# Performance work log

Hardware: AMD Instinct MI355X
Metric: run time of the kernel (lower is better)

Reference implementation:

```python
import jax, jax.numpy as jnp
import numpy as np

D_MODEL = 256
N_HEADS = 8
D_FFN = 1024
B, N = 4, 1024
HEAD_DIM = D_MODEL // N_HEADS
LN_EPS = 1e-5


def _ln(x, g, b):
    mu = jnp.mean(x, axis=-1, keepdims=True)
    var = jnp.var(x, axis=-1, keepdims=True)
    return (x - mu) * jax.lax.rsqrt(var + LN_EPS) * g + b


def setup_inputs() -> dict:
    key = jax.random.key(0)
    ks = jax.random.split(key, 16)
    s = 0.02
    return {
        "embed": jax.random.normal(ks[0], (B, N, D_MODEL), jnp.float32),
        "refer_bbox": jax.random.uniform(ks[1], (B, N, 4), jnp.float32),
        "dist": jax.random.uniform(ks[2], (B, N, N), jnp.float32),
        "query_pos": jax.random.normal(ks[3], (B, N, D_MODEL), jnp.float32),
        "in_proj_w": jax.random.normal(ks[4], (3 * D_MODEL, D_MODEL), jnp.float32) * s,
        "in_proj_b": jnp.zeros((3 * D_MODEL,), jnp.float32),
        "out_w": jax.random.normal(ks[5], (D_MODEL, D_MODEL), jnp.float32) * s,
        "out_b": jnp.zeros((D_MODEL,), jnp.float32),
        "tau_w": jax.random.normal(ks[6], (N_HEADS, D_MODEL), jnp.float32) * s,
        "tau_b": jax.random.uniform(ks[7], (N_HEADS,), jnp.float32, 0.0, 2.0),
        "w1": jax.random.normal(ks[8], (D_FFN, D_MODEL), jnp.float32) * s,
        "b1": jnp.zeros((D_FFN,), jnp.float32),
        "w2": jax.random.normal(ks[9], (D_MODEL, D_FFN), jnp.float32) * s,
        "b2": jnp.zeros((D_MODEL,), jnp.float32),
        "g1": jnp.ones((D_MODEL,), jnp.float32),
        "beta1": jnp.zeros((D_MODEL,), jnp.float32),
        "g2": jnp.ones((D_MODEL,), jnp.float32),
        "beta2": jnp.zeros((D_MODEL,), jnp.float32),
    }


def reference(embed, refer_bbox, dist, query_pos, in_proj_w, in_proj_b, out_w, out_b,
              tau_w, tau_b, w1, b1, w2, b2, g1, beta1, g2, beta2):
    # tau: (B, N, H) -> (B, H, N); additive bias mask[b,h,i,j] = dist[b,i,j] * tau[b,h,i]
    tau = (embed @ tau_w.T + tau_b).transpose(0, 2, 1)
    bias = dist[:, None, :, :] * tau[..., None]  # (B, H, N, N)

    qk = embed + query_pos  # q = k = embed + pos, v = embed
    wq, wk, wv = jnp.split(in_proj_w, 3, axis=0)
    bq, bk, bv = jnp.split(in_proj_b, 3, axis=0)
    q = (qk @ wq.T + bq).reshape(B, N, N_HEADS, HEAD_DIM)
    k = (qk @ wk.T + bk).reshape(B, N, N_HEADS, HEAD_DIM)
    v = (embed @ wv.T + bv).reshape(B, N, N_HEADS, HEAD_DIM)

    scores = jnp.einsum("bihd,bjhd->bhij", q, k) / np.sqrt(HEAD_DIM) + bias
    attn = jax.nn.softmax(scores, axis=-1)
    ctx = jnp.einsum("bhij,bjhd->bihd", attn, v).reshape(B, N, D_MODEL)
    tgt = ctx @ out_w.T + out_b

    x = _ln(embed + tgt, g1, beta1)
    ffn = jax.nn.relu(x @ w1.T + b1) @ w2.T + b2
    return _ln(x + ffn, g2, beta2)
```

## Files before the change

### kernel.cpp

```cpp
#include <hip/hip_runtime.h>
#include <math.h>

#define D_MODEL 256
#define N_HEADS 8
#define HEAD_DIM 32
#define D_FFN   1024
#define BB      4
#define NN      1024
#define M_TOT   (BB * NN)
#define LN_EPS  1e-5f

#define QSCALE_LOG2E 0.2550348612f
#define LOG2E        1.4426950408889634f

typedef float f32x4 __attribute__((ext_vector_type(4)));
typedef short bf16x8 __attribute__((ext_vector_type(8)));

__device__ __forceinline__ unsigned short f2bf(float f) {
    unsigned int u = __float_as_uint(f);
    unsigned int r = (u + 0x7fffu + ((u >> 16) & 1u)) >> 16;
    return (unsigned short)r;
}
__device__ __forceinline__ ushort4 pack4(float4 v) {
    ushort4 o; o.x = f2bf(v.x); o.y = f2bf(v.y); o.z = f2bf(v.z); o.w = f2bf(v.w);
    return o;
}
__device__ __forceinline__ float fast_exp2(float x) {
#if __has_builtin(__builtin_amdgcn_exp2f)
    return __builtin_amdgcn_exp2f(x);
#else
    return exp2f(x);
#endif
}

__global__ __launch_bounds__(256)
void prep_all_kernel(const float4* __restrict__ e, const float4* __restrict__ qp,
                     ushort4* __restrict__ ebf, ushort4* __restrict__ qkbf,
                     const float4* __restrict__ inw, const float4* __restrict__ outw,
                     const float4* __restrict__ w1, const float4* __restrict__ w2,
                     const float4* __restrict__ tauw,
                     ushort4* __restrict__ o_inw, ushort4* __restrict__ o_outw,
                     ushort4* __restrict__ o_w1, ushort4* __restrict__ o_w2,
                     ushort4* __restrict__ o_taupad) {
    if (blockIdx.x < 1024) {
        int i = blockIdx.x * 256 + threadIdx.x;
        float4 ev = e[i], pv = qp[i];
        ebf[i] = pack4(ev);
        float4 s = make_float4(ev.x + pv.x, ev.y + pv.y, ev.z + pv.z, ev.w + pv.w);
        qkbf[i] = pack4(s);
    } else {
        int i = (blockIdx.x - 1024) * 256 + threadIdx.x;
        if (i < 49152)       o_inw[i] = pack4(inw[i]);
        else if (i < 65536)  o_outw[i - 49152] = pack4(outw[i - 49152]);
        else if (i < 131072) o_w1[i - 65536] = pack4(w1[i - 65536]);
        else if (i < 196608) o_w2[i - 131072] = pack4(w2[i - 131072]);
        else if (i < 200704) {
            int q = i - 196608;
            if (q < 512) o_taupad[q] = pack4(tauw[q]);
            else { ushort4 z = {0, 0, 0, 0}; o_taupad[q] = z; }
        }
    }
}

__global__ __launch_bounds__(256)
void qkv_mfma_kernel(const unsigned short* __restrict__ qk_bf,
                     const unsigned short* __restrict__ emb_bf,
                     const unsigned short* __restrict__ inw_bf,
                     const unsigned short* __restrict__ taupad,
                     const float* __restrict__ in_proj_b, const float* __restrict__ tau_b,
                     unsigned short* __restrict__ qb, unsigned short* __restrict__ kb,
                     unsigned short* __restrict__ vbT, float* __restrict__ taub) {
    const int w    = threadIdx.x >> 6;
    const int lane = threadIdx.x & 63;
    const int l16 = lane & 15, l4 = lane >> 4;
    const int n0 = blockIdx.x * 64;
    const int m0 = blockIdx.y * 64;
    const int wm = (w >> 1) * 32, wn = (w & 1) * 32;

    const unsigned short* A = (blockIdx.x < 8) ? qk_bf : emb_bf;
    const unsigned short* W0 = (n0 < 768) ? &inw_bf[(size_t)(n0 + wn + l16) * D_MODEL]
                                          : &taupad[(size_t)(wn + l16) * D_MODEL];
    const unsigned short* Ar0 = &A[(size_t)(m0 + wm + l16) * D_MODEL];

    f32x4 acc[2][2] = {};
    #pragma unroll
    for (int k0 = 0; k0 < D_MODEL; k0 += 32) {
        bf16x8 a0 = *(const bf16x8*)&Ar0[k0 + l4 * 8];
        bf16x8 a1 = *(const bf16x8*)&Ar0[16 * D_MODEL + k0 + l4 * 8];
        bf16x8 b0 = *(const bf16x8*)&W0[k0 + l4 * 8];
        bf16x8 b1 = *(const bf16x8*)&W0[16 * D_MODEL + k0 + l4 * 8];
        acc[0][0] = __builtin_amdgcn_mfma_f32_16x16x32_bf16(a0, b0, acc[0][0], 0, 0, 0);
        acc[0][1] = __builtin_amdgcn_mfma_f32_16x16x32_bf16(a0, b1, acc[0][1], 0, 0, 0);
        acc[1][0] = __builtin_amdgcn_mfma_f32_16x16x32_bf16(a1, b0, acc[1][0], 0, 0, 0);
        acc[1][1] = __builtin_amdgcn_mfma_f32_16x16x32_bf16(a1, b1, acc[1][1], 0, 0, 0);
    }

    #pragma unroll
    for (int i = 0; i < 2; i++) {
        #pragma unroll
        for (int j = 0; j < 2; j++) {
            #pragma unroll
            for (int r = 0; r < 4; r++) {
                const int m = m0 + wm + i * 16 + l4 * 4 + r;
                const int b = m >> 10, nrow = m & 1023;
                const int c = n0 + wn + j * 16 + l16;
                float v = acc[i][j][r];
                if (c < 256) {
                    v = (v + in_proj_b[c]) * QSCALE_LOG2E;
                    int h = c >> 5, d = c & 31;
                    qb[((size_t)(b * N_HEADS + h) * NN + nrow) * HEAD_DIM + d] = f2bf(v);
                } else if (c < 512) {
                    v += in_proj_b[c];
                    int cc = c - 256; int h = cc >> 5, d = cc & 31;
                    kb[((size_t)(b * N_HEADS + h) * NN + nrow) * HEAD_DIM + d] = f2bf(v);
                } else if (c < 768) {
                    v += in_proj_b[c];
                    int cc = c - 512; int h = cc >> 5, d = cc & 31;
                    vbT[((size_t)(b * N_HEADS + h) * HEAD_DIM + d) * NN + nrow] = f2bf(v);
                } else if (c < 776) {
                    v = (v + tau_b[c - 768]) * LOG2E;
                    taub[(size_t)(b * N_HEADS + (c - 768)) * NN + nrow] = v;
                }
            }
        }
    }
}

__global__ __launch_bounds__(256)
void attn_mfma_kernel(const unsigned short* __restrict__ qb,
                      const unsigned short* __restrict__ kb,
                      const unsigned short* __restrict__ vbT,
                      const float* __restrict__ taub,
                      const float* __restrict__ dist,
                      float* __restrict__ Opart,
                      float* __restrict__ lpart) {
    __shared__ unsigned short Plds[4][16 * 72];
    const int w    = threadIdx.x >> 6;
    const int lane = threadIdx.x & 63;
    const int l16  = lane & 15;
    const int l4   = lane >> 4;
    const int bh = blockIdx.y;
    const int b = bh >> 3;
    const int z = blockIdx.z;
    const int i0 = blockIdx.x * 64 + w * 16;
    const int jbase = z * 256;

    const f32x4 zero = {0.f, 0.f, 0.f, 0.f};
    bf16x8 qf = *(const bf16x8*)&qb[((size_t)bh * NN + i0 + l16) * HEAD_DIM + l4 * 8];

    float tau_r[4];
    const float* drow[4];
    #pragma unroll
    for (int r = 0; r < 4; r++) {
        tau_r[r] = taub[(size_t)bh * NN + i0 + l4 * 4 + r];
        drow[r] = &dist[((size_t)b * NN + i0 + l4 * 4 + r) * NN];
    }

    float l_acc[4] = {0.f, 0.f, 0.f, 0.f};
    f32x4 O0 = zero, O1 = zero;

    unsigned short* pw = &Plds[w][0];
    const unsigned short* kbase = &kb[(size_t)bh * NN * HEAD_DIM];
    const unsigned short* vbase = &vbT[(size_t)bh * HEAD_DIM * NN];

    bf16x8 kf[4];
    float dd[4][4];
    #pragma unroll
    for (int s = 0; s < 4; s++)
        kf[s] = *(const bf16x8*)&kbase[(size_t)(jbase + s * 16 + l16) * HEAD_DIM + l4 * 8];
    #pragma unroll
    for (int s = 0; s < 4; s++)
        #pragma unroll
        for (int r = 0; r < 4; r++)
            dd[s][r] = drow[r][jbase + s * 16 + l16];

    for (int kt = 0; kt < 4; kt++) {
        const int j0 = jbase + kt * 64;
        bf16x8 vf[2][2];
        #pragma unroll
        for (int c = 0; c < 2; c++) {
            vf[c][0] = *(const bf16x8*)&vbase[(size_t)l16 * NN + j0 + c * 32 + l4 * 8];
            vf[c][1] = *(const bf16x8*)&vbase[(size_t)(16 + l16) * NN + j0 + c * 32 + l4 * 8];
        }
        bf16x8 kf_n[4];
        float dd_n[4][4];
        if (kt < 3) {
            const int j1 = j0 + 64;
            #pragma unroll
            for (int s = 0; s < 4; s++)
                kf_n[s] = *(const bf16x8*)&kbase[(size_t)(j1 + s * 16 + l16) * HEAD_DIM + l4 * 8];
            #pragma unroll
            for (int s = 0; s < 4; s++)
                #pragma unroll
                for (int r = 0; r < 4; r++)
                    dd_n[s][r] = drow[r][j1 + s * 16 + l16];
        }

        float parr[4][4];
        #pragma unroll
        for (int s = 0; s < 4; s++) {
            f32x4 S = __builtin_amdgcn_mfma_f32_16x16x32_bf16(qf, kf[s], zero, 0, 0, 0);
            #pragma unroll
            for (int r = 0; r < 4; r++) {
                const float p = fast_exp2(S[r] + dd[s][r] * tau_r[r]);
                parr[s][r] = p;
                l_acc[r] += p;
            }
        }

        #pragma unroll
        for (int s = 0; s < 4; s++)
            #pragma unroll
            for (int r = 0; r < 4; r++)
                pw[(l4 * 4 + r) * 72 + s * 16 + l16] = f2bf(parr[s][r]);
        asm volatile("s_waitcnt lgkmcnt(0)" ::: "memory");
        #pragma unroll
        for (int c = 0; c < 2; c++) {
            bf16x8 pf = *(const bf16x8*)&pw[l16 * 72 + c * 32 + l4 * 8];
            O0 = __builtin_amdgcn_mfma_f32_16x16x32_bf16(pf, vf[c][0], O0, 0, 0, 0);
            O1 = __builtin_amdgcn_mfma_f32_16x16x32_bf16(pf, vf[c][1], O1, 0, 0, 0);
        }

        if (kt < 3) {
            #pragma unroll
            for (int s = 0; s < 4; s++) {
                kf[s] = kf_n[s];
                #pragma unroll
                for (int r = 0; r < 4; r++) dd[s][r] = dd_n[s][r];
            }
        }
    }

    #pragma unroll
    for (int msk = 1; msk < 16; msk <<= 1)
        #pragma unroll
        for (int r = 0; r < 4; r++)
            l_acc[r] += __shfl_xor(l_acc[r], msk, 16);

    #pragma unroll
    for (int r = 0; r < 4; r++) {
        const int i = i0 + l4 * 4 + r;
        float* crow = &Opart[((size_t)(z * 32 + bh) * NN + i) * 32];
        crow[l16]      = O0[r];
        crow[16 + l16] = O1[r];
        if (l16 == 0)
            lpart[(size_t)(z * 32 + bh) * NN + i] = l_acc[r];
    }
}

__global__ __launch_bounds__(512)
void post_kernel(const float* __restrict__ Opart, const float* __restrict__ lpart,
                 const unsigned short* __restrict__ outw,
                 const float* __restrict__ out_b, const float* __restrict__ embed,
                 const float* __restrict__ g1, const float* __restrict__ beta1,
                 const unsigned short* __restrict__ w1, const float* __restrict__ b1,
                 const unsigned short* __restrict__ w2, const float* __restrict__ b2,
                 const float* __restrict__ g2, const float* __restrict__ beta2,
                 float* __restrict__ out) {
    __shared__ float Lh[16][8];
    __shared__ unsigned short cs[16][264];
    __shared__ unsigned short xs[16][264];
    __shared__ unsigned short fs[16][1032];
    __shared__ float sums[8][4][4][2];

    const int tid = threadIdx.x;
    const int w = tid >> 6, lane = tid & 63;
    const int l16 = lane & 15, l4 = lane >> 4;
    const int m0 = blockIdx.x * 16;
    const int b = m0 >> 10;

    if (tid < 128) {
        const int row = tid >> 3, h = tid & 7;
        const int i = (m0 + row) & 1023;
        const int rowA = ((b * 8 + h) << 10) + i;
        float l = 0.f;
        #pragma unroll
        for (int z = 0; z < 4; z++) l += lpart[z * 32768 + rowA];
        Lh[row][h] = 1.0f / l;
    }
    __syncthreads();

    {
        const int row = tid >> 5;
        const int d0 = (tid & 31) * 8;
        const int h = d0 >> 5;
        const int dd = d0 & 31;
        const int i = (m0 + row) & 1023;
        const int rowA = ((b * 8 + h) << 10) + i;
        f32x4 s0 = {0.f, 0.f, 0.f, 0.f}, s1 = {0.f, 0.f, 0.f, 0.f};
        #pragma unroll
        for (int z = 0; z < 4; z++) {
            const float* u = &Opart[((size_t)(z * 32768 + rowA)) * 32 + dd];
            s0 += *(const f32x4*)u;
            s1 += *(const f32x4*)(u + 4);
        }
        const float li = Lh[row][h];
        #pragma unroll
        for (int j = 0; j < 4; j++) {
            cs[row][d0 + j]     = f2bf(s0[j] * li);
            cs[row][d0 + 4 + j] = f2bf(s1[j] * li);
        }
    }
    __syncthreads();

    f32x4 accA[2] = {};
    #pragma unroll
    for (int k0 = 0; k0 < D_MODEL; k0 += 32) {
        bf16x8 a = *(const bf16x8*)&cs[l16][k0 + l4 * 8];
        #pragma unroll
        for (int j = 0; j < 2; j++) {
            const int c = w * 32 + j * 16 + l16;
            bf16x8 bj = *(const bf16x8*)&outw[(size_t)c * D_MODEL + k0 + l4 * 8];
            accA[j] = __builtin_amdgcn_mfma_f32_16x16x32_bf16(a, bj, accA[j], 0, 0, 0);
        }
    }
    float xv[2][4];
    {
        float s_r[4] = {0.f, 0.f, 0.f, 0.f}, q_r[4] = {0.f, 0.f, 0.f, 0.f};
        #pragma unroll
        for (int j = 0; j < 2; j++) {
            const int c = w * 32 + j * 16 + l16;
            const float bs = out_b[c];
            #pragma unroll
            for (int r = 0; r < 4; r++) {
                const int m = m0 + l4 * 4 + r;
                const float t = accA[j][r] + bs + embed[(size_t)m * D_MODEL + c];
                xv[j][r] = t; s_r[r] += t; q_r[r] += t * t;
            }
        }
        #pragma unroll
        for (int msk = 1; msk < 16; msk <<= 1)
            #pragma unroll
            for (int r = 0; r < 4; r++) {
                s_r[r] += __shfl_xor(s_r[r], msk, 16);
                q_r[r] += __shfl_xor(q_r[r], msk, 16);
            }
        if (l16 == 0)
            #pragma unroll
            for (int r = 0; r < 4; r++) {
                sums[w][l4][r][0] = s_r[r];
                sums[w][l4][r][1] = q_r[r];
            }
    }
    __syncthreads();
    #pragma unroll
    for (int r = 0; r < 4; r++) {
        float s = 0.f, q = 0.f;
        #pragma unroll
        for (int ww = 0; ww < 8; ww++) { s += sums[ww][l4][r][0]; q += sums[ww][l4][r][1]; }
        const float mu = s * (1.0f / D_MODEL);
        const float var = q * (1.0f / D_MODEL) - mu * mu;
        const float rstd = rsqrtf(var + LN_EPS);
        #pragma unroll
        for (int j = 0; j < 2; j++) {
            const int c = w * 32 + j * 16 + l16;
            const float ov = (xv[j][r] - mu) * rstd * g1[c] + beta1[c];
            xv[j][r] = ov;
            xs[l4 * 4 + r][c] = f2bf(ov);
        }
    }
    __syncthreads();

    f32x4 accB[8] = {};
    #pragma unroll
    for (int k0 = 0; k0 < D_MODEL; k0 += 32) {
        bf16x8 a = *(const bf16x8*)&xs[l16][k0 + l4 * 8];
        #pragma unroll
        for (int j = 0; j < 8; j++) {
            const int fc = w * 128 + j * 16 + l16;
            bf16x8 bj = *(const bf16x8*)&w1[(size_t)fc * D_MODEL + k0 + l4 * 8];
            accB[j] = __builtin_amdgcn_mfma_f32_16x16x32_bf16(a, bj, accB[j], 0, 0, 0);
        }
    }
    #pragma unroll
    for (int j = 0; j < 8; j++) {
        const int fc = w * 128 + j * 16 + l16;
        const float bs = b1[fc];
        #pragma unroll
        for (int r = 0; r < 4; r++)
            fs[l4 * 4 + r][fc] = f2bf(fmaxf(accB[j][r] + bs, 0.f));
    }
    __syncthreads();

    f32x4 accC[2] = {};
    #pragma unroll 8
    for (int k0 = 0; k0 < D_FFN; k0 += 32) {
        bf16x8 a = *(const bf16x8*)&fs[l16][k0 + l4 * 8];
        #pragma unroll
        for (int j = 0; j < 2; j++) {
            const int c = w * 32 + j * 16 + l16;
            bf16x8 bj = *(const bf16x8*)&w2[(size_t)c * D_FFN + k0 + l4 * 8];
            accC[j] = __builtin_amdgcn_mfma_f32_16x16x32_bf16(a, bj, accC[j], 0, 0, 0);
        }
    }
    float v2[2][4];
    {
        float s_r[4] = {0.f, 0.f, 0.f, 0.f}, q_r[4] = {0.f, 0.f, 0.f, 0.f};
        #pragma unroll
        for (int j = 0; j < 2; j++) {
            const int c = w * 32 + j * 16 + l16;
            const float bs = b2[c];
            #pragma unroll
            for (int r = 0; r < 4; r++) {
                const float t = accC[j][r] + bs + xv[j][r];
                v2[j][r] = t; s_r[r] += t; q_r[r] += t * t;
            }
        }
        #pragma unroll
        for (int msk = 1; msk < 16; msk <<= 1)
            #pragma unroll
            for (int r = 0; r < 4; r++) {
                s_r[r] += __shfl_xor(s_r[r], msk, 16);
                q_r[r] += __shfl_xor(q_r[r], msk, 16);
            }
        if (l16 == 0)
            #pragma unroll
            for (int r = 0; r < 4; r++) {
                sums[w][l4][r][0] = s_r[r];
                sums[w][l4][r][1] = q_r[r];
            }
    }
    __syncthreads();
    #pragma unroll
    for (int r = 0; r < 4; r++) {
        float s = 0.f, q = 0.f;
        #pragma unroll
        for (int ww = 0; ww < 8; ww++) { s += sums[ww][l4][r][0]; q += sums[ww][l4][r][1]; }
        const float mu = s * (1.0f / D_MODEL);
        const float var = q * (1.0f / D_MODEL) - mu * mu;
        const float rstd = rsqrtf(var + LN_EPS);
        const int m = m0 + l4 * 4 + r;
        #pragma unroll
        for (int j = 0; j < 2; j++) {
            const int c = w * 32 + j * 16 + l16;
            out[(size_t)m * D_MODEL + c] = (v2[j][r] - mu) * rstd * g2[c] + beta2[c];
        }
    }
}

extern "C" void kernel_launch(void* const* d_in, const int* in_sizes, int n_in,
                              void* d_out, int out_size, void* d_ws, size_t ws_size,
                              hipStream_t stream) {
    const float* embed     = (const float*)d_in[0];
    const float* dist      = (const float*)d_in[2];
    const float* query_pos = (const float*)d_in[3];
    const float* in_proj_w = (const float*)d_in[4];
    const float* in_proj_b = (const float*)d_in[5];
    const float* out_w     = (const float*)d_in[6];
    const float* out_b     = (const float*)d_in[7];
    const float* tau_w     = (const float*)d_in[8];
    const float* tau_b     = (const float*)d_in[9];
    const float* w1        = (const float*)d_in[10];
    const float* b1        = (const float*)d_in[11];
    const float* w2        = (const float*)d_in[12];
    const float* b2        = (const float*)d_in[13];
    const float* g1        = (const float*)d_in[14];
    const float* beta1     = (const float*)d_in[15];
    const float* g2        = (const float*)d_in[16];
    const float* beta2     = (const float*)d_in[17];
    float* out = (float*)d_out;

    char* ws = (char*)d_ws;
    const size_t MB = 1024 * 1024;
    const size_t KB = 1024;
    unsigned short* emb_bf  = (unsigned short*)(ws);
    unsigned short* qk_bf   = (unsigned short*)(ws + 2 * MB);
    unsigned short* qb      = (unsigned short*)(ws + 4 * MB);
    unsigned short* kb      = (unsigned short*)(ws + 6 * MB);
    unsigned short* vbT     = (unsigned short*)(ws + 8 * MB);
    float*          taub    = (float*)(ws + 10 * MB);
    unsigned short* inw_bf  = (unsigned short*)(ws + 11 * MB);
    unsigned short* outw_bf = (unsigned short*)(ws + 11 * MB + 512 * KB);
    unsigned short* w1_bf   = (unsigned short*)(ws + 12 * MB);
    unsigned short* w2_bf   = (unsigned short*)(ws + 12 * MB + 512 * KB);
    unsigned short* taupad  = (unsigned short*)(ws + 13 * MB);
    float*          Opart   = (float*)(ws + 14 * MB);
    float*          lpart   = (float*)(ws + 30 * MB);

    prep_all_kernel<<<dim3(1808), dim3(256), 0, stream>>>(
        (const float4*)embed, (const float4*)query_pos,
        (ushort4*)emb_bf, (ushort4*)qk_bf,
        (const float4*)in_proj_w, (const float4*)out_w, (const float4*)w1,
        (const float4*)w2, (const float4*)tau_w,
        (ushort4*)inw_bf, (ushort4*)outw_bf, (ushort4*)w1_bf, (ushort4*)w2_bf,
        (ushort4*)taupad);

    qkv_mfma_kernel<<<dim3(13, M_TOT / 64), dim3(256), 0, stream>>>(
        qk_bf, emb_bf, inw_bf, taupad, in_proj_b, tau_b, qb, kb, vbT, taub);

    attn_mfma_kernel<<<dim3(NN / 64, BB * N_HEADS, 4), dim3(256), 0, stream>>>(
        qb, kb, vbT, taub, dist, Opart, lpart);

    post_kernel<<<dim3(M_TOT / 16), dim3(512), 0, stream>>>(
        Opart, lpart, outw_bf, out_b, embed, g1, beta1,
        w1_bf, b1, w2_bf, b2, g2, beta2, out);
}
```

Measured before the change: 194.4 us.

## Fuse activation bf16 conversion into QKV GEMM, stage K/V in LDS, halve post tile

The separate embed/query_pos to bf16 pass is removed, and the QKV GEMM now reads fp32 activations and converts (and adds query_pos) in registers. The attention kernel cooperatively stages its K and V tiles in shared memory and permutes key order so the dist loads become vectorized float4, which drops the register double-buffering. The post kernel now processes 8 rows per block instead of 16, doubling the grid, and splits the K loops into two accumulators. The QKV GEMM converts redundantly across column blocks, and the 8-row post tile wastes half of each MFMA while re-reading the weights twice as often.

```diff
diff --git a/kernel.cpp b/kernel.cpp
--- a/kernel.cpp
+++ b/kernel.cpp
@@ -32,39 +32,46 @@
     return exp2f(x);
 #endif
 }
+__device__ __forceinline__ bf16x8 cvt8(const float* p) {
+    f32x4 x0 = *(const f32x4*)p, x1 = *(const f32x4*)(p + 4);
+    union { unsigned short s[8]; bf16x8 v; } u;
+    #pragma unroll
+    for (int j = 0; j < 4; j++) { u.s[j] = f2bf(x0[j]); u.s[4 + j] = f2bf(x1[j]); }
+    return u.v;
+}
+__device__ __forceinline__ bf16x8 cvt8_add(const float* p, const float* q) {
+    f32x4 x0 = *(const f32x4*)p, x1 = *(const f32x4*)(p + 4);
+    f32x4 y0 = *(const f32x4*)q, y1 = *(const f32x4*)(q + 4);
+    union { unsigned short s[8]; bf16x8 v; } u;
+    #pragma unroll
+    for (int j = 0; j < 4; j++) {
+        u.s[j] = f2bf(x0[j] + y0[j]);
+        u.s[4 + j] = f2bf(x1[j] + y1[j]);
+    }
+    return u.v;
+}
 
 __global__ __launch_bounds__(256)
-void prep_all_kernel(const float4* __restrict__ e, const float4* __restrict__ qp,
-                     ushort4* __restrict__ ebf, ushort4* __restrict__ qkbf,
-                     const float4* __restrict__ inw, const float4* __restrict__ outw,
-                     const float4* __restrict__ w1, const float4* __restrict__ w2,
-                     const float4* __restrict__ tauw,
-                     ushort4* __restrict__ o_inw, ushort4* __restrict__ o_outw,
-                     ushort4* __restrict__ o_w1, ushort4* __restrict__ o_w2,
-                     ushort4* __restrict__ o_taupad) {
-    if (blockIdx.x < 1024) {
-        int i = blockIdx.x * 256 + threadIdx.x;
-        float4 ev = e[i], pv = qp[i];
-        ebf[i] = pack4(ev);
-        float4 s = make_float4(ev.x + pv.x, ev.y + pv.y, ev.z + pv.z, ev.w + pv.w);
-        qkbf[i] = pack4(s);
-    } else {
-        int i = (blockIdx.x - 1024) * 256 + threadIdx.x;
-        if (i < 49152)       o_inw[i] = pack4(inw[i]);
-        else if (i < 65536)  o_outw[i - 49152] = pack4(outw[i - 49152]);
-        else if (i < 131072) o_w1[i - 65536] = pack4(w1[i - 65536]);
-        else if (i < 196608) o_w2[i - 131072] = pack4(w2[i - 131072]);
-        else if (i < 200704) {
-            int q = i - 196608;
-            if (q < 512) o_taupad[q] = pack4(tauw[q]);
-            else { ushort4 z = {0, 0, 0, 0}; o_taupad[q] = z; }
-        }
+void prep_w_kernel(const float4* __restrict__ inw, const float4* __restrict__ outw,
+                   const float4* __restrict__ w1, const float4* __restrict__ w2,
+                   const float4* __restrict__ tauw,
+                   ushort4* __restrict__ o_inw, ushort4* __restrict__ o_outw,
+                   ushort4* __restrict__ o_w1, ushort4* __restrict__ o_w2,
+                   ushort4* __restrict__ o_taupad) {
+    int i = blockIdx.x * 256 + threadIdx.x;
+    if (i < 49152)       o_inw[i] = pack4(inw[i]);
+    else if (i < 65536)  o_outw[i - 49152] = pack4(outw[i - 49152]);
+    else if (i < 131072) o_w1[i - 65536] = pack4(w1[i - 65536]);
+    else if (i < 196608) o_w2[i - 131072] = pack4(w2[i - 131072]);
+    else if (i < 200704) {
+        int q = i - 196608;
+        if (q < 512) o_taupad[q] = pack4(tauw[q]);
+        else { ushort4 z = {0, 0, 0, 0}; o_taupad[q] = z; }
     }
 }
 
 __global__ __launch_bounds__(256)
-void qkv_mfma_kernel(const unsigned short* __restrict__ qk_bf,
-                     const unsigned short* __restrict__ emb_bf,
+void qkv_mfma_kernel(const float* __restrict__ embed, const float* __restrict__ qpos,
                      const unsigned short* __restrict__ inw_bf,
                      const unsigned short* __restrict__ taupad,
                      const float* __restrict__ in_proj_b, const float* __restrict__ tau_b,
@@ -76,17 +83,21 @@
     const int n0 = blockIdx.x * 64;
     const int m0 = blockIdx.y * 64;
     const int wm = (w >> 1) * 32, wn = (w & 1) * 32;
-
-    const unsigned short* A = (blockIdx.x < 8) ? qk_bf : emb_bf;
+    const bool isqk = (blockIdx.x < 8);
+
+    const float* A0 = &embed[(size_t)(m0 + wm + l16) * D_MODEL];
+    const float* A1 = A0 + 16 * D_MODEL;
+    const float* P0 = &qpos[(size_t)(m0 + wm + l16) * D_MODEL];
+    const float* P1 = P0 + 16 * D_MODEL;
     const unsigned short* W0 = (n0 < 768) ? &inw_bf[(size_t)(n0 + wn + l16) * D_MODEL]
                                           : &taupad[(size_t)(wn + l16) * D_MODEL];
-    const unsigned short* Ar0 = &A[(size_t)(m0 + wm + l16) * D_MODEL];
 
     f32x4 acc[2][2] = {};
     #pragma unroll
     for (int k0 = 0; k0 < D_MODEL; k0 += 32) {
-        bf16x8 a0 = *(const bf16x8*)&Ar0[k0 + l4 * 8];
-        bf16x8 a1 = *(const bf16x8*)&Ar0[16 * D_MODEL + k0 + l4 * 8];
+        const int k = k0 + l4 * 8;
+        bf16x8 a0 = isqk ? cvt8_add(&A0[k], &P0[k]) : cvt8(&A0[k]);
+        bf16x8 a1 = isqk ? cvt8_add(&A1[k], &P1[k]) : cvt8(&A1[k]);
         bf16x8 b0 = *(const bf16x8*)&W0[k0 + l4 * 8];
         bf16x8 b1 = *(const bf16x8*)&W0[16 * D_MODEL + k0 + l4 * 8];
         acc[0][0] = __builtin_amdgcn_mfma_f32_16x16x32_bf16(a0, b0, acc[0][0], 0, 0, 0);
@@ -134,6 +145,8 @@
                       const float* __restrict__ dist,
                       float* __restrict__ Opart,
                       float* __restrict__ lpart) {
+    __shared__ unsigned short Kf[4][4][512];
+    __shared__ unsigned short Vf[4][2][2][512];
     __shared__ unsigned short Plds[4][16 * 72];
     const int w    = threadIdx.x >> 6;
     const int lane = threadIdx.x & 63;
@@ -145,89 +158,74 @@
     const int i0 = blockIdx.x * 64 + w * 16;
     const int jbase = z * 256;
 
+    {
+        const int kt = w;
+        const unsigned short* kb_z = &kb[((size_t)bh * NN + jbase + kt * 64) * HEAD_DIM];
+        #pragma unroll
+        for (int s = 0; s < 4; s++) {
+            bf16x8 kv = *(const bf16x8*)&kb_z[(size_t)(l16 * 4 + s) * HEAD_DIM + l4 * 8];
+            *(bf16x8*)&Kf[kt][s][lane * 8] = kv;
+        }
+        const unsigned short* vb_z = &vbT[(size_t)bh * HEAD_DIM * NN + jbase + kt * 64];
+        #pragma unroll
+        for (int c = 0; c < 2; c++)
+            #pragma unroll
+            for (int h2 = 0; h2 < 2; h2++) {
+                bf16x8 vv = *(const bf16x8*)&vb_z[(size_t)(h2 * 16 + l16) * NN + c * 32 + l4 * 8];
+                *(bf16x8*)&Vf[kt][c][h2][lane * 8] = vv;
+            }
+    }
+
     const f32x4 zero = {0.f, 0.f, 0.f, 0.f};
     bf16x8 qf = *(const bf16x8*)&qb[((size_t)bh * NN + i0 + l16) * HEAD_DIM + l4 * 8];
-
     float tau_r[4];
     const float* drow[4];
     #pragma unroll
     for (int r = 0; r < 4; r++) {
         tau_r[r] = taub[(size_t)bh * NN + i0 + l4 * 4 + r];
-        drow[r] = &dist[((size_t)b * NN + i0 + l4 * 4 + r) * NN];
-    }
-
+        drow[r] = &dist[((size_t)b * NN + i0 + l4 * 4 + r) * NN + jbase];
+    }
     float l_acc[4] = {0.f, 0.f, 0.f, 0.f};
     f32x4 O0 = zero, O1 = zero;
-
     unsigned short* pw = &Plds[w][0];
-    const unsigned short* kbase = &kb[(size_t)bh * NN * HEAD_DIM];
-    const unsigned short* vbase = &vbT[(size_t)bh * HEAD_DIM * NN];
-
-    bf16x8 kf[4];
-    float dd[4][4];
-    #pragma unroll
-    for (int s = 0; s < 4; s++)
-        kf[s] = *(const bf16x8*)&kbase[(size_t)(jbase + s * 16 + l16) * HEAD_DIM + l4 * 8];
-    #pragma unroll
-    for (int s = 0; s < 4; s++)
+
+    __syncthreads();
+
+    for (int kt = 0; kt < 4; kt++) {
+        const int j0 = kt * 64;
+        f32x4 dd4[4];
         #pragma unroll
         for (int r = 0; r < 4; r++)
-            dd[s][r] = drow[r][jbase + s * 16 + l16];
-
-    for (int kt = 0; kt < 4; kt++) {
-        const int j0 = jbase + kt * 64;
-        bf16x8 vf[2][2];
-        #pragma unroll
-        for (int c = 0; c < 2; c++) {
-            vf[c][0] = *(const bf16x8*)&vbase[(size_t)l16 * NN + j0 + c * 32 + l4 * 8];
-            vf[c][1] = *(const bf16x8*)&vbase[(size_t)(16 + l16) * NN + j0 + c * 32 + l4 * 8];
-        }
-        bf16x8 kf_n[4];
-        float dd_n[4][4];
-        if (kt < 3) {
-            const int j1 = j0 + 64;
-            #pragma unroll
-            for (int s = 0; s < 4; s++)
-                kf_n[s] = *(const bf16x8*)&kbase[(size_t)(j1 + s * 16 + l16) * HEAD_DIM + l4 * 8];
-            #pragma unroll
-            for (int s = 0; s < 4; s++)
-                #pragma unroll
-                for (int r = 0; r < 4; r++)
-                    dd_n[s][r] = drow[r][j1 + s * 16 + l16];
-        }
+            dd4[r] = *(const f32x4*)&drow[r][j0 + l16 * 4];
 
         float parr[4][4];
         #pragma unroll
         for (int s = 0; s < 4; s++) {
-            f32x4 S = __builtin_amdgcn_mfma_f32_16x16x32_bf16(qf, kf[s], zero, 0, 0, 0);
-            #pragma unroll
-            for (int r = 0; r < 4; r++) {
-                const float p = fast_exp2(S[r] + dd[s][r] * tau_r[r]);
+            bf16x8 kfr = *(const bf16x8*)&Kf[kt][s][lane * 8];
+            f32x4 S = __builtin_amdgcn_mfma_f32_16x16x32_bf16(qf, kfr, zero, 0, 0, 0);
+            #pragma unroll
+            for (int r = 0; r < 4; r++) {
+                const float p = fast_exp2(S[r] + dd4[r][s] * tau_r[r]);
                 parr[s][r] = p;
                 l_acc[r] += p;
             }
         }
 
         #pragma unroll
-        for (int s = 0; s < 4; s++)
-            #pragma unroll
-            for (int r = 0; r < 4; r++)
-                pw[(l4 * 4 + r) * 72 + s * 16 + l16] = f2bf(parr[s][r]);
+        for (int r = 0; r < 4; r++) {
+            ushort4 pk;
+            pk.x = f2bf(parr[0][r]); pk.y = f2bf(parr[1][r]);
+            pk.z = f2bf(parr[2][r]); pk.w = f2bf(parr[3][r]);
+            *(ushort4*)&pw[(l4 * 4 + r) * 72 + l16 * 4] = pk;
+        }
         asm volatile("s_waitcnt lgkmcnt(0)" ::: "memory");
         #pragma unroll
         for (int c = 0; c < 2; c++) {
             bf16x8 pf = *(const bf16x8*)&pw[l16 * 72 + c * 32 + l4 * 8];
-            O0 = __builtin_amdgcn_mfma_f32_16x16x32_bf16(pf, vf[c][0], O0, 0, 0, 0);
-            O1 = __builtin_amdgcn_mfma_f32_16x16x32_bf16(pf, vf[c][1], O1, 0, 0, 0);
-        }
-
-        if (kt < 3) {
-            #pragma unroll
-            for (int s = 0; s < 4; s++) {
-                kf[s] = kf_n[s];
-                #pragma unroll
-                for (int r = 0; r < 4; r++) dd[s][r] = dd_n[s][r];
-            }
+            bf16x8 v0 = *(const bf16x8*)&Vf[kt][c][0][lane * 8];
+            bf16x8 v1 = *(const bf16x8*)&Vf[kt][c][1][lane * 8];
+            O0 = __builtin_amdgcn_mfma_f32_16x16x32_bf16(pf, v0, O0, 0, 0, 0);
+            O1 = __builtin_amdgcn_mfma_f32_16x16x32_bf16(pf, v1, O1, 0, 0, 0);
         }
     }
 
@@ -257,19 +255,22 @@
                  const unsigned short* __restrict__ w2, const float* __restrict__ b2,
                  const float* __restrict__ g2, const float* __restrict__ beta2,
                  float* __restrict__ out) {
-    __shared__ float Lh[16][8];
-    __shared__ unsigned short cs[16][264];
-    __shared__ unsigned short xs[16][264];
-    __shared__ unsigned short fs[16][1032];
-    __shared__ float sums[8][4][4][2];
+    __shared__ float Lh[8][8];
+    __shared__ unsigned short cs[8][264];
+    __shared__ unsigned short xs[8][264];
+    __shared__ unsigned short fs[8][1032];
+    __shared__ float sums[8][2][4][2];
 
     const int tid = threadIdx.x;
     const int w = tid >> 6, lane = tid & 63;
     const int l16 = lane & 15, l4 = lane >> 4;
-    const int m0 = blockIdx.x * 16;
+    const int m0 = blockIdx.x * 8;
     const int b = m0 >> 10;
-
-    if (tid < 128) {
+    const int row8 = l16 & 7;
+    const bool vrow = (l4 < 2);
+    const int mr = m0 + (l4 & 1) * 4;
+
+    if (tid < 64) {
         const int row = tid >> 3, h = tid & 7;
         const int i = (m0 + row) & 1023;
         const int rowA = ((b * 8 + h) << 10) + i;
@@ -280,11 +281,10 @@
     }
     __syncthreads();
 
-    {
+    if (tid < 256) {
         const int row = tid >> 5;
         const int d0 = (tid & 31) * 8;
-        const int h = d0 >> 5;
-        const int dd = d0 & 31;
+        const int h = d0 >> 5, dd = d0 & 31;
         const int i = (m0 + row) & 1023;
         const int rowA = ((b * 8 + h) << 10) + i;
         f32x4 s0 = {0.f, 0.f, 0.f, 0.f}, s1 = {0.f, 0.f, 0.f, 0.f};
@@ -303,15 +303,19 @@
     }
     __syncthreads();
 
-    f32x4 accA[2] = {};
-    #pragma unroll
-    for (int k0 = 0; k0 < D_MODEL; k0 += 32) {
-        bf16x8 a = *(const bf16x8*)&cs[l16][k0 + l4 * 8];
+    f32x4 accA[2][2] = {};
+    #pragma unroll
+    for (int kk = 0; kk < 4; kk++) {
+        const int ka = kk * 32, kb2 = 128 + kk * 32;
+        bf16x8 x0 = *(const bf16x8*)&cs[row8][ka + l4 * 8];
+        bf16x8 x1 = *(const bf16x8*)&cs[row8][kb2 + l4 * 8];
         #pragma unroll
         for (int j = 0; j < 2; j++) {
             const int c = w * 32 + j * 16 + l16;
-            bf16x8 bj = *(const bf16x8*)&outw[(size_t)c * D_MODEL + k0 + l4 * 8];
-            accA[j] = __builtin_amdgcn_mfma_f32_16x16x32_bf16(a, bj, accA[j], 0, 0, 0);
+            bf16x8 b0 = *(const bf16x8*)&outw[(size_t)c * D_MODEL + ka + l4 * 8];
+            bf16x8 b1v = *(const bf16x8*)&outw[(size_t)c * D_MODEL + kb2 + l4 * 8];
+            accA[j][0] = __builtin_amdgcn_mfma_f32_16x16x32_bf16(x0, b0, accA[j][0], 0, 0, 0);
+            accA[j][1] = __builtin_amdgcn_mfma_f32_16x16x32_bf16(x1, b1v, accA[j][1], 0, 0, 0);
         }
     }
     float xv[2][4];
@@ -323,8 +327,8 @@
             const float bs = out_b[c];
             #pragma unroll
             for (int r = 0; r < 4; r++) {
-                const int m = m0 + l4 * 4 + r;
-                const float t = accA[j][r] + bs + embed[(size_t)m * D_MODEL + c];
+                const float t = accA[j][0][r] + accA[j][1][r] + bs
+                              + embed[(size_t)(mr + r) * D_MODEL + c];
                 xv[j][r] = t; s_r[r] += t; q_r[r] += t * t;
             }
         }
@@ -335,7 +339,7 @@
                 s_r[r] += __shfl_xor(s_r[r], msk, 16);
                 q_r[r] += __shfl_xor(q_r[r], msk, 16);
             }
-        if (l16 == 0)
+        if (l16 == 0 && vrow)
             #pragma unroll
             for (int r = 0; r < 4; r++) {
                 sums[w][l4][r][0] = s_r[r];
@@ -343,20 +347,22 @@
             }
     }
     __syncthreads();
-    #pragma unroll
-    for (int r = 0; r < 4; r++) {
-        float s = 0.f, q = 0.f;
-        #pragma unroll
-        for (int ww = 0; ww < 8; ww++) { s += sums[ww][l4][r][0]; q += sums[ww][l4][r][1]; }
-        const float mu = s * (1.0f / D_MODEL);
-        const float var = q * (1.0f / D_MODEL) - mu * mu;
-        const float rstd = rsqrtf(var + LN_EPS);
-        #pragma unroll
-        for (int j = 0; j < 2; j++) {
-            const int c = w * 32 + j * 16 + l16;
-            const float ov = (xv[j][r] - mu) * rstd * g1[c] + beta1[c];
-            xv[j][r] = ov;
-            xs[l4 * 4 + r][c] = f2bf(ov);
+    if (vrow) {
+        #pragma unroll
+        for (int r = 0; r < 4; r++) {
+            float s = 0.f, q = 0.f;
+            #pragma unroll
+            for (int ww = 0; ww < 8; ww++) { s += sums[ww][l4][r][0]; q += sums[ww][l4][r][1]; }
+            const float mu = s * (1.0f / D_MODEL);
+            const float var = q * (1.0f / D_MODEL) - mu * mu;
+            const float rstd = rsqrtf(var + LN_EPS);
+            #pragma unroll
+            for (int j = 0; j < 2; j++) {
+                const int c = w * 32 + j * 16 + l16;
+                const float ov = (xv[j][r] - mu) * rstd * g1[c] + beta1[c];
+                xv[j][r] = ov;
+                xs[l4 * 4 + r][c] = f2bf(ov);
+            }
         }
     }
     __syncthreads();
@@ -364,7 +370,7 @@
     f32x4 accB[8] = {};
     #pragma unroll
     for (int k0 = 0; k0 < D_MODEL; k0 += 32) {
-        bf16x8 a = *(const bf16x8*)&xs[l16][k0 + l4 * 8];
+        bf16x8 a = *(const bf16x8*)&xs[row8][k0 + l4 * 8];
         #pragma unroll
         for (int j = 0; j < 8; j++) {
             const int fc = w * 128 + j * 16 + l16;
@@ -372,25 +378,32 @@
             accB[j] = __builtin_amdgcn_mfma_f32_16x16x32_bf16(a, bj, accB[j], 0, 0, 0);
         }
     }
-    #pragma unroll
-    for (int j = 0; j < 8; j++) {
-        const int fc = w * 128 + j * 16 + l16;
-        const float bs = b1[fc];
-        #pragma unroll
-        for (int r = 0; r < 4; r++)
-            fs[l4 * 4 + r][fc] = f2bf(fmaxf(accB[j][r] + bs, 0.f));
-    }
-    __syncthreads();
-
-    f32x4 accC[2] = {};
-    #pragma unroll 8
-    for (int k0 = 0; k0 < D_FFN; k0 += 32) {
-        bf16x8 a = *(const bf16x8*)&fs[l16][k0 + l4 * 8];
+    if (vrow) {
+        #pragma unroll
+        for (int j = 0; j < 8; j++) {
+            const int fc = w * 128 + j * 16 + l16;
+            const float bs = b1[fc];
+            #pragma unroll
+            for (int r = 0; r < 4; r++)
+                fs[l4 * 4 + r][fc] = f2bf(fmaxf(accB[j][r] + bs, 0.f));
+        }
+    }
+    __syncthreads();
+
+    f32x4 accC[2][2] = {};
+    #pragma unroll
+    for (int kk = 0; kk < 16; kk++) {
+        const int ka = kk * 32, kb2 = 512 + kk * 32;
+        bf16x8 f0 = *(const bf16x8*)&fs[row8][ka + l4 * 8];
+        bf16x8 f1 = *(const bf16x8*)&fs[row8][kb2 + l4 * 8];
         #pragma unroll
         for (int j = 0; j < 2; j++) {
             const int c = w * 32 + j * 16 + l16;
-            bf16x8 bj = *(const bf16x8*)&w2[(size_t)c * D_FFN + k0 + l4 * 8];
-            accC[j] = __builtin_amdgcn_mfma_f32_16x16x32_bf16(a, bj, accC[j], 0, 0, 0);
+            const unsigned short* wr = &w2[(size_t)c * D_FFN];
+            bf16x8 b0 = *(const bf16x8*)&wr[ka + l4 * 8];
+            bf16x8 b1v = *(const bf16x8*)&wr[kb2 + l4 * 8];
+            accC[j][0] = __builtin_amdgcn_mfma_f32_16x16x32_bf16(f0, b0, accC[j][0], 0, 0, 0);
+            accC[j][1] = __builtin_amdgcn_mfma_f32_16x16x32_bf16(f1, b1v, accC[j][1], 0, 0, 0);
         }
     }
     float v2[2][4];
@@ -402,7 +415,7 @@
             const float bs = b2[c];
             #pragma unroll
             for (int r = 0; r < 4; r++) {
-                const float t = accC[j][r] + bs + xv[j][r];
+                const float t = accC[j][0][r] + accC[j][1][r] + bs + xv[j][r];
                 v2[j][r] = t; s_r[r] += t; q_r[r] += t * t;
             }
         }
@@ -413,7 +426,7 @@
                 s_r[r] += __shfl_xor(s_r[r], msk, 16);
                 q_r[r] += __shfl_xor(q_r[r], msk, 16);
             }
-        if (l16 == 0)
+        if (l16 == 0 && vrow)
             #pragma unroll
             for (int r = 0; r < 4; r++) {
                 sums[w][l4][r][0] = s_r[r];
@@ -421,19 +434,20 @@
             }
     }
     __syncthreads();
-    #pragma unroll
-    for (int r = 0; r < 4; r++) {
-        float s = 0.f, q = 0.f;
-        #pragma unroll
-        for (int ww = 0; ww < 8; ww++) { s += sums[ww][l4][r][0]; q += sums[ww][l4][r][1]; }
-        const float mu = s * (1.0f / D_MODEL);
-        const float var = q * (1.0f / D_MODEL) - mu * mu;
-        const float rstd = rsqrtf(var + LN_EPS);
-        const int m = m0 + l4 * 4 + r;
-        #pragma unroll
-        for (int j = 0; j < 2; j++) {
-            const int c = w * 32 + j * 16 + l16;
-            out[(size_t)m * D_MODEL + c] = (v2[j][r] - mu) * rstd * g2[c] + beta2[c];
+    if (vrow) {
+        #pragma unroll
+        for (int r = 0; r < 4; r++) {
+            float s = 0.f, q = 0.f;
+            #pragma unroll
+            for (int ww = 0; ww < 8; ww++) { s += sums[ww][l4][r][0]; q += sums[ww][l4][r][1]; }
+            const float mu = s * (1.0f / D_MODEL);
+            const float var = q * (1.0f / D_MODEL) - mu * mu;
+            const float rstd = rsqrtf(var + LN_EPS);
+            #pragma unroll
+            for (int j = 0; j < 2; j++) {
+                const int c = w * 32 + j * 16 + l16;
+                out[(size_t)(mr + r) * D_MODEL + c] = (v2[j][r] - mu) * rstd * g2[c] + beta2[c];
+            }
         }
     }
 }
@@ -463,35 +477,31 @@
     char* ws = (char*)d_ws;
     const size_t MB = 1024 * 1024;
     const size_t KB = 1024;
-    unsigned short* emb_bf  = (unsigned short*)(ws);
-    unsigned short* qk_bf   = (unsigned short*)(ws + 2 * MB);
-    unsigned short* qb      = (unsigned short*)(ws + 4 * MB);
-    unsigned short* kb      = (unsigned short*)(ws + 6 * MB);
-    unsigned short* vbT     = (unsigned short*)(ws + 8 * MB);
-    float*          taub    = (float*)(ws + 10 * MB);
-    unsigned short* inw_bf  = (unsigned short*)(ws + 11 * MB);
-    unsigned short* outw_bf = (unsigned short*)(ws + 11 * MB + 512 * KB);
-    unsigned short* w1_bf   = (unsigned short*)(ws + 12 * MB);
-    unsigned short* w2_bf   = (unsigned short*)(ws + 12 * MB + 512 * KB);
-    unsigned short* taupad  = (unsigned short*)(ws + 13 * MB);
-    float*          Opart   = (float*)(ws + 14 * MB);
-    float*          lpart   = (float*)(ws + 30 * MB);
-
-    prep_all_kernel<<<dim3(1808), dim3(256), 0, stream>>>(
-        (const float4*)embed, (const float4*)query_pos,
-        (ushort4*)emb_bf, (ushort4*)qk_bf,
+    unsigned short* qb      = (unsigned short*)(ws);
+    unsigned short* kb      = (unsigned short*)(ws + 2 * MB);
+    unsigned short* vbT     = (unsigned short*)(ws + 4 * MB);
+    float*          taub    = (float*)(ws + 6 * MB);
+    unsigned short* inw_bf  = (unsigned short*)(ws + 7 * MB);
+    unsigned short* outw_bf = (unsigned short*)(ws + 7 * MB + 512 * KB);
+    unsigned short* w1_bf   = (unsigned short*)(ws + 8 * MB);
+    unsigned short* w2_bf   = (unsigned short*)(ws + 8 * MB + 512 * KB);
+    unsigned short* taupad  = (unsigned short*)(ws + 9 * MB);
+    float*          Opart   = (float*)(ws + 10 * MB);
+    float*          lpart   = (float*)(ws + 26 * MB);
+
+    prep_w_kernel<<<dim3(784), dim3(256), 0, stream>>>(
         (const float4*)in_proj_w, (const float4*)out_w, (const float4*)w1,
         (const float4*)w2, (const float4*)tau_w,
         (ushort4*)inw_bf, (ushort4*)outw_bf, (ushort4*)w1_bf, (ushort4*)w2_bf,
         (ushort4*)taupad);
 
     qkv_mfma_kernel<<<dim3(13, M_TOT / 64), dim3(256), 0, stream>>>(
-        qk_bf, emb_bf, inw_bf, taupad, in_proj_b, tau_b, qb, kb, vbT, taub);
+        embed, query_pos, inw_bf, taupad, in_proj_b, tau_b, qb, kb, vbT, taub);
 
     attn_mfma_kernel<<<dim3(NN / 64, BB * N_HEADS, 4), dim3(256), 0, stream>>>(
         qb, kb, vbT, taub, dist, Opart, lpart);
 
-    post_kernel<<<dim3(M_TOT / 16), dim3(512), 0, stream>>>(
+    post_kernel<<<dim3(M_TOT / 8), dim3(512), 0, stream>>>(
         Opart, lpart, outw_bf, out_b, embed, g1, beta1,
         w1_bf, b1, w2_bf, b2, g2, beta2, out);
 }
```

After: 228.9 us. +17.7%, slower.
